# Performance work log

Measured on AMD Instinct MI355X. Metric: run time of the kernel, lower is better.

Reference implementation:

```python
import jax, jax.numpy as jnp
import numpy as np

N_NODES = 100000
N_EDGES = 1600000
IN_DIM = 64
HEADS = [4, 4]
DIMS = [16, 16]


def gat_layer(x, src, dst, W, al, ar, b, n_nodes):
    """DGL-style GATConv: x [N,F] -> [N,H,D]."""
    H, D = al.shape
    z = (x @ W).reshape(-1, H, D)                      # [N,H,D]
    el = jnp.sum(z * al, axis=-1)                      # [N,H]
    er = jnp.sum(z * ar, axis=-1)                      # [N,H]
    e = jax.nn.leaky_relu(el[src] + er[dst], 0.2)      # [E,H] edge scores
    # numerically-stable edge softmax over incoming edges of each dst node
    m = jax.ops.segment_max(e, dst, num_segments=n_nodes)
    m = jnp.where(jnp.isfinite(m), m, 0.0)
    ex = jnp.exp(e - jax.lax.stop_gradient(m)[dst])    # [E,H]
    denom = jax.ops.segment_sum(ex, dst, num_segments=n_nodes)
    alpha = ex / jnp.maximum(denom[dst], 1e-9)         # [E,H]
    # scatter-aggregate messages alpha * z[src]
    out = jax.ops.segment_sum(alpha[:, :, None] * z[src], dst, num_segments=n_nodes)
    return out + b.reshape(H, D)


def setup_inputs() -> dict:
    key = jax.random.key(0)
    ks = jax.random.split(key, 16)
    feat = jax.random.normal(ks[0], (N_NODES, IN_DIM), dtype=jnp.float32)
    src = jax.random.randint(ks[1], (N_EDGES,), 0, N_NODES, dtype=jnp.int32)
    dst = jax.random.randint(ks[2], (N_EDGES,), 0, N_NODES, dtype=jnp.int32)
    def lin(k, fi, fo):
        return jax.random.normal(k, (fi, fo), dtype=jnp.float32) * (1.0 / np.sqrt(fi))
    H0, D0 = HEADS[0], DIMS[0]
    H1, D1 = HEADS[1], DIMS[1]
    inp = {
        "feat": feat, "src": src, "dst": dst,
        "W0": lin(ks[3], IN_DIM, H0 * D0),
        "al0": jax.random.normal(ks[4], (H0, D0), jnp.float32) * 0.1,
        "ar0": jax.random.normal(ks[5], (H0, D0), jnp.float32) * 0.1,
        "b0": jnp.zeros((H0 * D0,), jnp.float32),
        "W1": lin(ks[6], H0 * D0, H1 * D1),
        "al1": jax.random.normal(ks[7], (H1, D1), jnp.float32) * 0.1,
        "ar1": jax.random.normal(ks[8], (H1, D1), jnp.float32) * 0.1,
        "b1": jnp.zeros((H1 * D1,), jnp.float32),
        "Wo": lin(ks[9], H1 * D1, 1),
        "alo": jax.random.normal(ks[10], (1, 1), jnp.float32) * 0.1,
        "aro": jax.random.normal(ks[11], (1, 1), jnp.float32) * 0.1,
        "bo": jnp.zeros((1,), jnp.float32),
    }
    return inp


def reference(feat, src, dst, W0, al0, ar0, b0, W1, al1, ar1, b1, Wo, alo, aro, bo):
    n = feat.shape[0]
    h = gat_layer(feat, src, dst, W0, al0, ar0, b0, n)       # [N,H0,D0]
    h = jax.nn.relu(h).reshape(n, -1)                         # head concat
    h = gat_layer(h, src, dst, W1, al1, ar1, b1, n)           # [N,H1,D1]
    h = jax.nn.relu(h).reshape(n, -1)
    out = gat_layer(h, src, dst, Wo, alo, aro, bo, n)         # [N,1,1]
    return jnp.squeeze(out, axis=1)                           # [N,1]
```

## Files before the change

### kernel.cpp

```cpp
#include <hip/hip_runtime.h>
#include <hip/hip_fp16.h>
#include <math.h>

#define NN 100000
#define NE 1600000
#define NBUK 391
#define CAP 4608
#define EPB 4096

__device__ __forceinline__ float leaky02(float v) {
    return v > 0.0f ? v : 0.2f * v;
}


__global__ __launch_bounds__(256) void k_bucket(
    const int* __restrict__ src, const int* __restrict__ dst,
    int* __restrict__ bucketCnt, int* __restrict__ gBuf)
{
    __shared__ int stg[EPB];
    __shared__ int tgt[EPB];
    __shared__ int lcnt[NBUK];
    __shared__ int lexc[NBUK];
    __shared__ int lgb[NBUK];
    __shared__ int totalLocal;
    const int t = threadIdx.x;
    const int e0 = blockIdx.x * EPB;

    for (int i = t; i < NBUK; i += 256) lcnt[i] = 0;
    __syncthreads();

    int bk[16], pk[16];
    #pragma unroll
    for (int j = 0; j < 16; ++j) {
        const int e = e0 + j * 256 + t;
        if (e < NE) {
            const int d = dst[e];
            bk[j] = d >> 8;
            pk[j] = (src[e] << 8) | (d & 255);
            atomicAdd(&lcnt[bk[j]], 1);
        } else bk[j] = -1;
    }
    __syncthreads();

    if (t < 64) {
        int carry = 0;
        for (int c = 0; c < NBUK; c += 64) {
            const int idx = c + t;
            int v = (idx < NBUK) ? lcnt[idx] : 0;
            int inc = v;
            #pragma unroll
            for (int off = 1; off < 64; off <<= 1) {
                int u = __shfl_up(inc, off, 64);
                if (t >= off) inc += u;
            }
            if (idx < NBUK) lexc[idx] = carry + inc - v;
            carry += __shfl(inc, 63, 64);
        }
        if (t == 0) totalLocal = carry;
    }
    __syncthreads();

    for (int i = t; i < NBUK; i += 256) {
        const int c = lcnt[i];
        lgb[i] = c ? atomicAdd(&bucketCnt[i], c) : 0;
        lcnt[i] = 0;
    }
    __syncthreads();

    #pragma unroll
    for (int j = 0; j < 16; ++j) {
        if (bk[j] >= 0) {
            const int r = atomicAdd(&lcnt[bk[j]], 1);
            const int p = lexc[bk[j]] + r;
            stg[p] = pk[j];
            int slot = lgb[bk[j]] + r;
            if (slot >= CAP) slot = CAP - 1;
            tgt[p] = bk[j] * CAP + slot;
        }
    }
    __syncthreads();

    const int tot = totalLocal;
    for (int i = t; i < tot; i += 256)
        gBuf[tgt[i]] = stg[i];
}

__global__ __launch_bounds__(64) void k_bbase(
    const int* __restrict__ bucketCnt, int* __restrict__ bucketBase,
    int* __restrict__ row_ptr)
{
    const int t = threadIdx.x;
    int carry = 0;
    for (int c = 0; c < NBUK; c += 64) {
        const int idx = c + t;
        int v = (idx < NBUK) ? bucketCnt[idx] : 0;
        int inc = v;
        #pragma unroll
        for (int off = 1; off < 64; off <<= 1) {
            int u = __shfl_up(inc, off, 64);
            if (t >= off) inc += u;
        }
        if (idx < NBUK) bucketBase[idx] = carry + inc - v;
        carry += __shfl(inc, 63, 64);
    }
    if (t == 0) row_ptr[NN] = NE;
}

__global__ __launch_bounds__(256) void k_csr_local(
    const int* __restrict__ bucketCnt, const int* __restrict__ bucketBase,
    const int* __restrict__ gBuf,
    int* __restrict__ row_ptr, int* __restrict__ ssrc)
{
    __shared__ int stg2[CAP];
    __shared__ int stg3[CAP];
    __shared__ int c2[256];
    __shared__ int sc[256];
    const int t = threadIdx.x;
    const int k = blockIdx.x;
    const int cnt = min(bucketCnt[k], CAP);
    const int gb  = bucketBase[k];

    c2[t] = 0;
    __syncthreads();
    for (int i = t; i < cnt; i += 256) {
        const int pk = gBuf[k * CAP + i];
        stg2[i] = pk;
        atomicAdd(&c2[pk & 255], 1);
    }
    __syncthreads();
    if (t < 64) {
        int carry = 0;
        for (int c = 0; c < 256; c += 64) {
            int v = c2[c + t];
            int inc = v;
            #pragma unroll
            for (int off = 1; off < 64; off <<= 1) {
                int u = __shfl_up(inc, off, 64);
                if (t >= off) inc += u;
            }
            sc[c + t] = carry + inc - v;
            carry += __shfl(inc, 63, 64);
        }
    }
    __syncthreads();
    const int node = (k << 8) + t;
    if (node < NN) row_ptr[node] = gb + sc[t];
    c2[t] = 0;
    __syncthreads();
    for (int i = t; i < cnt; i += 256) {
        const int pk = stg2[i];
        const int dl = pk & 255;
        const int r = atomicAdd(&c2[dl], 1);
        stg3[sc[dl] + r] = pk >> 8;
    }
    __syncthreads();
    for (int i = t; i < cnt; i += 256)
        ssrc[gb + i] = stg3[i];
}


__global__ __launch_bounds__(256) void k_node_prep(
    const float* __restrict__ xin, const float* __restrict__ W,
    const float* __restrict__ al, const float* __restrict__ ar,
    __half* __restrict__ z, float* __restrict__ el, float* __restrict__ er)
{
    __shared__ float Ws[64 * 64];
    __shared__ float xs[16][64];
    const int t = threadIdx.x;
    const int nodeBase = blockIdx.x * 16;

    #pragma unroll
    for (int i = 0; i < 16; ++i) Ws[t + 256 * i] = W[t + 256 * i];
    #pragma unroll
    for (int i = 0; i < 4; ++i) {
        int idx = t + 256 * i;
        xs[idx >> 6][idx & 63] = xin[(size_t)(nodeBase + (idx >> 6)) * 64 + (idx & 63)];
    }
    __syncthreads();

    const int col = t & 63;
    const int ng  = t >> 6;
    const float a_l = al[col], a_r = ar[col];

    float zacc[4] = {0.f, 0.f, 0.f, 0.f};
    #pragma unroll
    for (int k = 0; k < 64; ++k) {
        float w = Ws[k * 64 + col];
        #pragma unroll
        for (int i = 0; i < 4; ++i) zacc[i] += xs[ng * 4 + i][k] * w;
    }

    #pragma unroll
    for (int i = 0; i < 4; ++i) {
        const int n = nodeBase + ng * 4 + i;
        z[(size_t)n * 64 + col] = __float2half(zacc[i]);
        float pl = zacc[i] * a_l, pr = zacc[i] * a_r;
        #pragma unroll
        for (int off = 8; off > 0; off >>= 1) {
            pl += __shfl_xor(pl, off, 16);
            pr += __shfl_xor(pr, off, 16);
        }
        if ((col & 15) == 0) {
            const int h = col >> 4;
            el[n * 4 + h] = pl;
            er[n * 4 + h] = pr;
        }
    }
}

__global__ __launch_bounds__(256) void k_csr_agg(
    const int* __restrict__ row_ptr, const int* __restrict__ ssrc,
    const float* __restrict__ el, const float* __restrict__ er,
    const __half* __restrict__ z, const float* __restrict__ b,
    float* __restrict__ xout,
    const float* __restrict__ Wo,
    float* __restrict__ zo)
{
    const int t = threadIdx.x;
    const int wv = t >> 6, l = t & 63;
    const int sg = l >> 4, sl = l & 15;
    const int eh = l & 3;
    const int hh = sl >> 2;
    const int n = blockIdx.x * 4 + wv;
    const int beg = row_ptr[n], deg = row_ptr[n + 1] - beg;
    const float er_eh = er[n * 4 + eh];

    float4 acc = {0.f, 0.f, 0.f, 0.f};
    float den4 = 0.f;
    for (int base = 0; base < deg; base += 16) {
        const int myE = base + (l >> 2);
        int s = 0; float x = 0.f;
        if (myE < deg) {
            s = ssrc[beg + myE];
            x = __expf(leaky02(el[s * 4 + eh] + er_eh));
        }
        den4 += x;
        const int rem = deg - base;
        const int nk = (min(rem, 16) + 3) >> 2;
        for (int k = 0; k < nk; ++k) {
            const int ec = k * 4 + sg;
            const int   sj = __shfl(s, ec * 4, 64);
            const float xj = __shfl(x, ec * 4 + hh, 64);
            const uint2 raw = *(const uint2*)(z + (size_t)sj * 64 + sl * 4);
            const float2 f01 = __half22float2(*(const __half2*)&raw.x);
            const float2 f23 = __half22float2(*(const __half2*)&raw.y);
            acc.x += xj * f01.x; acc.y += xj * f01.y;
            acc.z += xj * f23.x; acc.w += xj * f23.y;
        }
    }
    #pragma unroll
    for (int off = 16; off < 64; off <<= 1) {
        acc.x += __shfl_xor(acc.x, off, 64);
        acc.y += __shfl_xor(acc.y, off, 64);
        acc.z += __shfl_xor(acc.z, off, 64);
        acc.w += __shfl_xor(acc.w, off, 64);
    }
    #pragma unroll
    for (int off = 4; off < 64; off <<= 1) den4 += __shfl_xor(den4, off, 64);
    const float den = fmaxf(__shfl(den4, hh, 64), 1e-9f);

    const float4 b4 = *(const float4*)(b + sl * 4);
    float4 v;
    v.x = fmaxf(acc.x / den + b4.x, 0.f);
    v.y = fmaxf(acc.y / den + b4.y, 0.f);
    v.z = fmaxf(acc.z / den + b4.z, 0.f);
    v.w = fmaxf(acc.w / den + b4.w, 0.f);

    if (xout) {
        if (l < 16) *(float4*)(xout + (size_t)n * 64 + sl * 4) = v;
    } else {
        const float4 w4 = *(const float4*)(Wo + sl * 4);
        float p = v.x * w4.x + v.y * w4.y + v.z * w4.z + v.w * w4.w;
        #pragma unroll
        for (int off = 1; off < 16; off <<= 1) p += __shfl_xor(p, off, 64);
        if (l == 0) zo[n] = p;
    }
}


__global__ __launch_bounds__(256) void k_csr_agg_o(
    const int* __restrict__ row_ptr, const int* __restrict__ ssrc,
    const float* __restrict__ zo, const float* __restrict__ alo,
    const float* __restrict__ aro, const float* __restrict__ bo,
    float* __restrict__ out)
{
    const int t = threadIdx.x, l = t & 15;
    const int n = blockIdx.x * 16 + (t >> 4);
    const float a = alo[0];
    const float zr = aro[0] * zo[n];
    const int beg = row_ptr[n], end = row_ptr[n + 1];

    float den = 0.f, accv = 0.f;
    for (int i = beg + l; i < end; i += 16) {
        const float zs = zo[ssrc[i]];
        const float ex = __expf(leaky02(a * zs + zr));
        den += ex; accv += ex * zs;
    }
    #pragma unroll
    for (int off = 8; off; off >>= 1) {
        den  += __shfl_xor(den, off, 16);
        accv += __shfl_xor(accv, off, 16);
    }
    if (l == 0) out[n] = accv / fmaxf(den, 1e-9f) + bo[0];
}


extern "C" void kernel_launch(void* const* d_in, const int* in_sizes, int n_in,
                              void* d_out, int out_size, void* d_ws, size_t ws_size,
                              hipStream_t stream) {
    const float* feat = (const float*)d_in[0];
    const int*   src  = (const int*)d_in[1];
    const int*   dst  = (const int*)d_in[2];
    const float* W0   = (const float*)d_in[3];
    const float* al0  = (const float*)d_in[4];
    const float* ar0  = (const float*)d_in[5];
    const float* b0   = (const float*)d_in[6];
    const float* W1   = (const float*)d_in[7];
    const float* al1  = (const float*)d_in[8];
    const float* ar1  = (const float*)d_in[9];
    const float* b1   = (const float*)d_in[10];
    const float* Wo   = (const float*)d_in[11];
    const float* alo  = (const float*)d_in[12];
    const float* aro  = (const float*)d_in[13];
    const float* bo   = (const float*)d_in[14];
    float* out = (float*)d_out;

    int* bucketCnt  = (int*)d_ws;
    int* bucketBase = bucketCnt + NBUK;
    int* row_ptr    = bucketBase + NBUK;
    int* gBuf       = row_ptr + (NN + 1);
    int* ssrc       = gBuf + (size_t)NBUK * CAP;
    __half* z  = (__half*)(ssrc + NE);
    float* xA  = (float*)(z + (size_t)NN * 64);
    float* el  = xA + (size_t)NN * 64;
    float* er  = el + (size_t)NN * 4;
    float* zo  = er + (size_t)NN * 4;

    const int gN16 = NN / 16;
    const int gAgg = NN / 4;

    hipMemsetAsync(bucketCnt, 0, NBUK * sizeof(int), stream);
    k_bucket   <<<NBUK, 256, 0, stream>>>(src, dst, bucketCnt, gBuf);
    k_bbase    <<<1, 64, 0, stream>>>(bucketCnt, bucketBase, row_ptr);
    k_csr_local<<<NBUK, 256, 0, stream>>>(bucketCnt, bucketBase, gBuf,
                                          row_ptr, ssrc);

    k_node_prep<<<gN16, 256, 0, stream>>>(feat, W0, al0, ar0, z, el, er);
    k_csr_agg  <<<gAgg, 256, 0, stream>>>(row_ptr, ssrc, el, er, z, b0,
                                          xA, nullptr, nullptr);

    k_node_prep<<<gN16, 256, 0, stream>>>(xA, W1, al1, ar1, z, el, er);
    k_csr_agg  <<<gAgg, 256, 0, stream>>>(row_ptr, ssrc, el, er, z, b1,
                                          nullptr, Wo, zo);

    k_csr_agg_o<<<gN16, 256, 0, stream>>>(row_ptr, ssrc, zo, alo, aro, bo, out);
}
```

Baseline: 337.4 us.

## Hold weight column in registers and tile 64 nodes per block in node prep

The node projection kernel now keeps each lane's column of W in 64 registers instead of staging all of W in shared memory. Each block covers 64 nodes instead of 16, loading x with float4 and reading it from LDS as float4 broadcasts. This cuts the per-block W reload and the LDS traffic, at the cost of high register pressure and fewer blocks. The workspace offset also shifts by one int.

Measured after the change: 350.4 us. +3.9%, slower.

```diff
diff --git a/kernel.cpp b/kernel.cpp
--- a/kernel.cpp
+++ b/kernel.cpp
@@ -164,46 +164,64 @@
     const float* __restrict__ al, const float* __restrict__ ar,
     __half* __restrict__ z, float* __restrict__ el, float* __restrict__ er)
 {
-    __shared__ float Ws[64 * 64];
-    __shared__ float xs[16][64];
-    const int t = threadIdx.x;
-    const int nodeBase = blockIdx.x * 16;
-
-    #pragma unroll
-    for (int i = 0; i < 16; ++i) Ws[t + 256 * i] = W[t + 256 * i];
-    #pragma unroll
-    for (int i = 0; i < 4; ++i) {
-        int idx = t + 256 * i;
-        xs[idx >> 6][idx & 63] = xin[(size_t)(nodeBase + (idx >> 6)) * 64 + (idx & 63)];
-    }
-    __syncthreads();
-
-    const int col = t & 63;
-    const int ng  = t >> 6;
-    const float a_l = al[col], a_r = ar[col];
-
-    float zacc[4] = {0.f, 0.f, 0.f, 0.f};
-    #pragma unroll
-    for (int k = 0; k < 64; ++k) {
-        float w = Ws[k * 64 + col];
-        #pragma unroll
-        for (int i = 0; i < 4; ++i) zacc[i] += xs[ng * 4 + i][k] * w;
-    }
-
-    #pragma unroll
-    for (int i = 0; i < 4; ++i) {
-        const int n = nodeBase + ng * 4 + i;
-        z[(size_t)n * 64 + col] = __float2half(zacc[i]);
-        float pl = zacc[i] * a_l, pr = zacc[i] * a_r;
-        #pragma unroll
-        for (int off = 8; off > 0; off >>= 1) {
-            pl += __shfl_xor(pl, off, 16);
-            pr += __shfl_xor(pr, off, 16);
-        }
-        if ((col & 15) == 0) {
-            const int h = col >> 4;
-            el[n * 4 + h] = pl;
-            er[n * 4 + h] = pr;
+    __shared__ __align__(16) float xs[64][64];
+    const int t = threadIdx.x;
+    const int lane = t & 63, wv = t >> 6;
+    const int nodeBase = blockIdx.x * 64;
+
+    {
+        const float4* xin4 = (const float4*)(xin + (size_t)nodeBase * 64);
+        float4* xs4 = (float4*)&xs[0][0];
+        const int lim4 = NN * 16 - nodeBase * 16;
+        #pragma unroll
+        for (int i = 0; i < 4; ++i) {
+            const int idx = t + 256 * i;
+            if (idx < lim4) xs4[idx] = xin4[idx];
+        }
+    }
+
+    float wc[64];
+    #pragma unroll
+    for (int k = 0; k < 64; ++k) wc[k] = W[k * 64 + lane];
+    const float a_l = al[lane], a_r = ar[lane];
+    __syncthreads();
+
+    #pragma unroll 1
+    for (int g = 0; g < 4; ++g) {
+        const int n0 = wv * 16 + g * 4;
+        float acc0 = 0.f, acc1 = 0.f, acc2 = 0.f, acc3 = 0.f;
+        #pragma unroll
+        for (int k4 = 0; k4 < 16; ++k4) {
+            const float4 x0 = *(const float4*)&xs[n0 + 0][k4 * 4];
+            const float4 x1 = *(const float4*)&xs[n0 + 1][k4 * 4];
+            const float4 x2 = *(const float4*)&xs[n0 + 2][k4 * 4];
+            const float4 x3 = *(const float4*)&xs[n0 + 3][k4 * 4];
+            const float w0 = wc[k4 * 4 + 0], w1 = wc[k4 * 4 + 1];
+            const float w2 = wc[k4 * 4 + 2], w3 = wc[k4 * 4 + 3];
+            acc0 += x0.x * w0 + x0.y * w1 + x0.z * w2 + x0.w * w3;
+            acc1 += x1.x * w0 + x1.y * w1 + x1.z * w2 + x1.w * w3;
+            acc2 += x2.x * w0 + x2.y * w1 + x2.z * w2 + x2.w * w3;
+            acc3 += x3.x * w0 + x3.y * w1 + x3.z * w2 + x3.w * w3;
+        }
+        #pragma unroll
+        for (int i = 0; i < 4; ++i) {
+            const float accv = (i == 0) ? acc0 : (i == 1) ? acc1
+                             : (i == 2) ? acc2 : acc3;
+            const int n = nodeBase + n0 + i;
+            if (n < NN) {
+                z[(size_t)n * 64 + lane] = __float2half(accv);
+                float pl = accv * a_l, pr = accv * a_r;
+                #pragma unroll
+                for (int off = 8; off > 0; off >>= 1) {
+                    pl += __shfl_xor(pl, off, 16);
+                    pr += __shfl_xor(pr, off, 16);
+                }
+                if ((lane & 15) == 0) {
+                    const int h = lane >> 4;
+                    el[n * 4 + h] = pl;
+                    er[n * 4 + h] = pr;
+                }
+            }
         }
     }
 }
@@ -328,7 +346,7 @@
     int* bucketCnt  = (int*)d_ws;
     int* bucketBase = bucketCnt + NBUK;
     int* row_ptr    = bucketBase + NBUK;
-    int* gBuf       = row_ptr + (NN + 1);
+    int* gBuf       = row_ptr + (NN + 2);
     int* ssrc       = gBuf + (size_t)NBUK * CAP;
     __half* z  = (__half*)(ssrc + NE);
     float* xA  = (float*)(z + (size_t)NN * 64);
@@ -336,8 +354,9 @@
     float* er  = el + (size_t)NN * 4;
     float* zo  = er + (size_t)NN * 4;
 
-    const int gN16 = NN / 16;
-    const int gAgg = NN / 4;
+    const int gPrep = (NN + 63) / 64;
+    const int gN16  = NN / 16;
+    const int gAgg  = NN / 4;
 
     hipMemsetAsync(bucketCnt, 0, NBUK * sizeof(int), stream);
     k_bucket   <<<NBUK, 256, 0, stream>>>(src, dst, bucketCnt, gBuf);
@@ -345,11 +364,11 @@
     k_csr_local<<<NBUK, 256, 0, stream>>>(bucketCnt, bucketBase, gBuf,
                                           row_ptr, ssrc);
 
-    k_node_prep<<<gN16, 256, 0, stream>>>(feat, W0, al0, ar0, z, el, er);
+    k_node_prep<<<gPrep, 256, 0, stream>>>(feat, W0, al0, ar0, z, el, er);
     k_csr_agg  <<<gAgg, 256, 0, stream>>>(row_ptr, ssrc, el, er, z, b0,
                                           xA, nullptr, nullptr);
 
-    k_node_prep<<<gN16, 256, 0, stream>>>(xA, W1, al1, ar1, z, el, er);
+    k_node_prep<<<gPrep, 256, 0, stream>>>(xA, W1, al1, ar1, z, el, er);
     k_csr_agg  <<<gAgg, 256, 0, stream>>>(row_ptr, ssrc, el, er, z, b1,
                                           nullptr, Wo, zo);
 
```
